# Kernel tuning notes

Hardware: AMD Instinct MI355X
Metric: run time of the kernel (lower is better)

The kernel has to match this reference:

```python
import jax, jax.numpy as jnp
import numpy as np

N = 50000      # nodes
E = 800000     # edges (avg degree 16)
F0 = 128       # input features
F = 128        # per-layer out_features (layer output = 2F after alpha/beta concat)
M = 16         # n_machines
BN_EPS = 1e-3  # Keras BatchNormalization default epsilon


def setup_inputs() -> dict:
    key = jax.random.key(0)
    ks = jax.random.split(key, 12)
    x = jax.random.normal(ks[0], (N, F0), jnp.float32)
    adj_rows = jax.random.randint(ks[1], (E,), 0, N, jnp.int32)
    adj_cols = jax.random.randint(ks[2], (E,), 0, N, jnp.int32)
    adj_vals = jax.random.uniform(ks[3], (E,), jnp.float32)
    l0_Walpha = jax.random.normal(ks[4], (6, F0, F), jnp.float32) * 0.05
    l0_Wbeta = jax.random.normal(ks[5], (6, F0, F), jnp.float32) * 0.05
    l0_bn = jax.random.normal(ks[6], (4, F), jnp.float32)
    l1_Walpha = jax.random.normal(ks[7], (6, 2 * F, F), jnp.float32) * 0.05
    l1_Wbeta = jax.random.normal(ks[8], (6, 2 * F, F), jnp.float32) * 0.05
    l1_bn = jax.random.normal(ks[9], (4, F), jnp.float32)
    We = jax.random.normal(ks[10], (2 * F, M), jnp.float32) * 0.05
    be = jax.random.normal(ks[11], (M,), jnp.float32) * 0.05
    return dict(x=x, adj_rows=adj_rows, adj_cols=adj_cols, adj_vals=adj_vals,
                l0_Walpha=l0_Walpha, l0_Wbeta=l0_Wbeta, l0_bn=l0_bn,
                l1_Walpha=l1_Walpha, l1_Wbeta=l1_Wbeta, l1_bn=l1_bn,
                We=We, be=be)


def _spmm(rows, cols, vals, x):
    # y[r] = sum_{edges (r,c)} vals * x[c]  == sparse A @ x
    return jax.ops.segment_sum(vals[:, None] * x[cols], rows, num_segments=x.shape[0])


def _bn(h, gamma, beta):
    # Keras BatchNormalization(axis=1) on (N, F): per-feature stats over nodes (training mode)
    mu = jnp.mean(h, axis=0, keepdims=True)
    var = jnp.var(h, axis=0, keepdims=True)
    return gamma * (h - mu) * jax.lax.rsqrt(var + BN_EPS) + beta


def _gnn_layer(x, rows, cols, vals, Wa, Wb, bn):
    a0 = _spmm(rows, cols, vals, x)
    a1 = _spmm(rows, cols, vals, a0)
    a2 = _spmm(rows, cols, vals, _spmm(rows, cols, vals, a1))
    alpha = x @ (Wa[0] + Wa[1] + Wa[2]) + a0 @ Wa[3] + a1 @ Wa[4] + a2 @ Wa[5]
    alpha = _bn(jax.nn.relu(alpha), bn[0], bn[1])
    beta = x @ (Wb[0] + Wb[1] + Wb[2]) + a0 @ Wb[3] + a1 @ Wb[4] + a2 @ Wb[5]
    beta = _bn(beta, bn[2], bn[3])
    return jnp.concatenate((alpha, beta), axis=1)  # (N, 2F)


def reference(x, adj_rows, adj_cols, adj_vals,
              l0_Walpha, l0_Wbeta, l0_bn,
              l1_Walpha, l1_Wbeta, l1_bn,
              We, be):
    h = _gnn_layer(x, adj_rows, adj_cols, adj_vals, l0_Walpha, l0_Wbeta, l0_bn)
    h = _gnn_layer(h, adj_rows, adj_cols, adj_vals, l1_Walpha, l1_Wbeta, l1_bn)
    # EdgeDense: per-edge score per machine = adj_val * (z[row] + z[col])
    z = h @ We + be                                   # (N, M)
    scores = adj_vals[:, None] * (z[adj_rows] + z[adj_cols])  # (E, M)
    return jax.nn.softmax(scores, axis=1)
```

## Files before the change

kernel.cpp:

```cpp
#include <hip/hip_runtime.h>
#include <stdint.h>

#define NN 50000
#define NE 800000
#define NP 50048
#define SCANB 196

typedef _Float16 f16x8 __attribute__((ext_vector_type(8)));
typedef float f32x4 __attribute__((ext_vector_type(4)));

__device__ __forceinline__ float h2f(unsigned short u){
  union { unsigned short u; _Float16 h; } x; x.u = u; return (float)x.h;
}
__device__ __forceinline__ unsigned short f2h(float f){
  union { _Float16 h; unsigned short u; } x; x.h = (_Float16)f; return x.u;
}
__device__ __forceinline__ void load_lds16(const void* g, void* l){
  __builtin_amdgcn_global_load_lds((const __attribute__((address_space(1))) void*)g,
                                   (__attribute__((address_space(3))) void*)l, 16, 0, 0);
}

__global__ void k_cast(const float* __restrict__ src, unsigned short* __restrict__ dst, int n4){
  int i = blockIdx.x*blockDim.x + threadIdx.x;
  if (i >= n4) return;
  float4 v = ((const float4*)src)[i];
  uint2 o;
  o.x = (unsigned int)f2h(v.x) | ((unsigned int)f2h(v.y) << 16);
  o.y = (unsigned int)f2h(v.z) | ((unsigned int)f2h(v.w) << 16);
  ((uint2*)dst)[i] = o;
}

__global__ void k_hist(const int* __restrict__ rows, int* __restrict__ cnt){
  int e = blockIdx.x*blockDim.x + threadIdx.x;
  if (e < NE) atomicAdd(&cnt[rows[e]], 1);
}

__global__ void k_scan1(const int* __restrict__ cnt, int* __restrict__ rowptr, int* __restrict__ bsum){
  __shared__ int sh[256];
  int t = threadIdx.x, b = blockIdx.x;
  int idx = b * 256 + t;
  int v = (idx < NN) ? cnt[idx] : 0;
  sh[t] = v; __syncthreads();
  #pragma unroll
  for (int off = 1; off < 256; off <<= 1){
    int u = (t >= off) ? sh[t - off] : 0;
    __syncthreads();
    sh[t] += u;
    __syncthreads();
  }
  if (idx < NN) rowptr[idx] = sh[t] - v;
  if (t == 255) bsum[b] = sh[255];
}

__global__ void k_scan2(const int* __restrict__ bsum, int* __restrict__ boff){
  __shared__ int sh[256];
  int t = threadIdx.x;
  int v = (t < SCANB) ? bsum[t] : 0;
  sh[t] = v; __syncthreads();
  #pragma unroll
  for (int off = 1; off < 256; off <<= 1){
    int u = (t >= off) ? sh[t - off] : 0;
    __syncthreads();
    sh[t] += u;
    __syncthreads();
  }
  if (t < SCANB) boff[t] = sh[t] - v;
  if (t == SCANB) boff[SCANB] = sh[255];
}

__global__ void k_scan3(int* __restrict__ rowptr, const int* __restrict__ boff){
  int idx = blockIdx.x * 256 + threadIdx.x;
  if (idx < NN) rowptr[idx] += boff[idx >> 8];
  else if (idx == NN) rowptr[NN] = boff[SCANB];
}

__global__ void k_scatter(const int* __restrict__ rows, const int* __restrict__ cols,
                          const float* __restrict__ vals,
                          const int* __restrict__ rowptr, int* __restrict__ fill,
                          int* __restrict__ colss, float* __restrict__ valss){
  int e = blockIdx.x*blockDim.x + threadIdx.x;
  if (e >= NE) return;
  int r = rows[e];
  int p = rowptr[r] + atomicAdd(&fill[r], 1);
  colss[p] = cols[e];
  valss[p] = vals[e];
}

__global__ void k_buildWT(const float* __restrict__ Wa, const float* __restrict__ Wb,
                          unsigned short* __restrict__ WT, int Fin){
  int Ktot = 4 * Fin;
  int idx = blockIdx.x*blockDim.x + threadIdx.x;
  if (idx >= 256 * Ktot) return;
  int j = idx / Ktot, k = idx - j * Ktot;
  int seg = k / Fin, ki = k - seg * Fin;
  const float* W = (j < 128) ? Wa : Wb;
  int jj = (j < 128) ? j : j - 128;
  int stride = Fin * 128;
  float v;
  if (seg == 0)
    v = W[0*stride + ki*128 + jj] + W[1*stride + ki*128 + jj] + W[2*stride + ki*128 + jj];
  else
    v = W[(seg + 2)*stride + ki*128 + jj];
  WT[j*Ktot + k] = f2h(v);
}

template<int F>
__global__ void k_spmm(const int* __restrict__ rowptr, const int* __restrict__ colss,
                       const float* __restrict__ valss,
                       const unsigned short* __restrict__ X, unsigned short* __restrict__ Y){
  int row = blockIdx.x * (blockDim.x >> 6) + (threadIdx.x >> 6);
  if (row >= NN) return;
  int lane = threadIdx.x & 63;
  constexpr int P = F / 64;
  float acc[P];
  #pragma unroll
  for (int i = 0; i < P; i++) acc[i] = 0.f;
  int s = rowptr[row], e = rowptr[row + 1];
  for (int base = s; base < e; base += 64){
    int idx = base + lane;
    bool ok = idx < e;
    int   cc = ok ? colss[idx] : 0;
    float vv = ok ? valss[idx] : 0.f;
    int n = e - base; if (n > 64) n = 64;
    for (int jb = 0; jb < n; jb += 8){
      int cj[8]; float vj[8];
      #pragma unroll
      for (int u = 0; u < 8; u++){
        cj[u] = __shfl(cc, jb + u);
        vj[u] = __shfl(vv, jb + u);
      }
      if (P == 2){
        unsigned int g[8];
        #pragma unroll
        for (int u = 0; u < 8; u++)
          g[u] = *(const unsigned int*)(X + (size_t)cj[u] * F + lane * P);
        #pragma unroll
        for (int u = 0; u < 8; u++){
          acc[0] += vj[u] * h2f((unsigned short)g[u]);
          acc[1] += vj[u] * h2f((unsigned short)(g[u] >> 16));
        }
      } else {
        uint2 g[8];
        #pragma unroll
        for (int u = 0; u < 8; u++)
          g[u] = *(const uint2*)(X + (size_t)cj[u] * F + lane * P);
        #pragma unroll
        for (int u = 0; u < 8; u++){
          acc[0] += vj[u] * h2f((unsigned short)g[u].x);
          acc[1] += vj[u] * h2f((unsigned short)(g[u].x >> 16));
          acc[2] += vj[u] * h2f((unsigned short)g[u].y);
          acc[3] += vj[u] * h2f((unsigned short)(g[u].y >> 16));
        }
      }
    }
  }
  unsigned short* dst = Y + (size_t)row * F + lane * P;
  if (P == 2){
    unsigned int o = (unsigned int)f2h(acc[0]) | ((unsigned int)f2h(acc[1]) << 16);
    *(unsigned int*)dst = o;
  } else {
    uint2 o;
    o.x = (unsigned int)f2h(acc[0]) | ((unsigned int)f2h(acc[1]) << 16);
    o.y = (unsigned int)f2h(acc[2]) | ((unsigned int)f2h(acc[3]) << 16);
    *(uint2*)dst = o;
  }
}

template<int FIN>
__global__ __launch_bounds__(256) void k_gemm4(
    const unsigned short* __restrict__ A0, const unsigned short* __restrict__ A1,
    const unsigned short* __restrict__ A2, const unsigned short* __restrict__ A3,
    const unsigned short* __restrict__ BT, float* __restrict__ C){
  constexpr int KTOT = 4 * FIN;
  __shared__ unsigned short As[128 * 32];
  __shared__ unsigned short Bs[128 * 32];
  int tid = threadIdx.x, lane = tid & 63;
  int wm = (tid >> 6) & 1, wn = tid >> 7;
  int bm = blockIdx.x, bn = blockIdx.y;

  f32x4 acc[4][4];
  #pragma unroll
  for (int i = 0; i < 4; i++)
    #pragma unroll
    for (int j = 0; j < 4; j++) acc[i][j] = (f32x4){0.f, 0.f, 0.f, 0.f};

  int ac = (tid & 3) * 8;
  int gr0 = bm * 128 + (tid >> 2);        if (gr0 >= NN) gr0 = NN - 1;
  int gr1 = bm * 128 + ((256 + tid) >> 2); if (gr1 >= NN) gr1 = NN - 1;
  int br0 = (tid >> 2), br1 = ((256 + tid) >> 2);
  const unsigned short* Bb = BT + (size_t)(bn * 128) * KTOT;
  unsigned short* Adst0 = As + (size_t)(tid & ~63) * 8;
  unsigned short* Adst1 = As + (size_t)(256 + (tid & ~63)) * 8;
  unsigned short* Bdst0 = Bs + (size_t)(tid & ~63) * 8;
  unsigned short* Bdst1 = Bs + (size_t)(256 + (tid & ~63)) * 8;

  int m0 = wm * 64 + (lane & 15);
  int n0 = wn * 64 + (lane & 15);
  int qk = (lane >> 4) * 8;

  #pragma unroll
  for (int seg = 0; seg < 4; seg++){
    const unsigned short* Asrc = (seg == 0) ? A0 : (seg == 1) ? A1 : (seg == 2) ? A2 : A3;
    const unsigned short* Bseg = Bb + seg * FIN;
    for (int kl = 0; kl < FIN; kl += 32){
      load_lds16(Asrc + (size_t)gr0 * FIN + kl + ac, Adst0);
      load_lds16(Asrc + (size_t)gr1 * FIN + kl + ac, Adst1);
      load_lds16(Bseg + (size_t)br0 * KTOT + kl + ac, Bdst0);
      load_lds16(Bseg + (size_t)br1 * KTOT + kl + ac, Bdst1);
      __syncthreads();
      f16x8 af[4], bfr[4];
      #pragma unroll
      for (int i = 0; i < 4; i++) af[i]  = *(const f16x8*)(As + (m0 + i * 16) * 32 + qk);
      #pragma unroll
      for (int j = 0; j < 4; j++) bfr[j] = *(const f16x8*)(Bs + (n0 + j * 16) * 32 + qk);
      #pragma unroll
      for (int i = 0; i < 4; i++)
        #pragma unroll
        for (int j = 0; j < 4; j++)
          acc[i][j] = __builtin_amdgcn_mfma_f32_16x16x32_f16(af[i], bfr[j], acc[i][j], 0, 0, 0);
      __syncthreads();
    }
  }
  int cn = bn * 128 + wn * 64 + (lane & 15);
  int rb = bm * 128 + wm * 64 + ((lane >> 4) << 2);
  #pragma unroll
  for (int i = 0; i < 4; i++)
    #pragma unroll
    for (int j = 0; j < 4; j++)
      #pragma unroll
      for (int g = 0; g < 4; g++){
        int rr = rb + i * 16 + g;
        if (rr < NN) C[(size_t)rr * 256 + cn + j * 16] = acc[i][j][g];
      }
}

__global__ void k_bnstats(const float* __restrict__ H, float* __restrict__ stats){
  int j = threadIdx.x;
  float s = 0.f, s2 = 0.f;
  for (int r = blockIdx.x; r < NN; r += gridDim.x){
    float v = H[(size_t)r * 256 + j];
    if (j < 128) v = fmaxf(v, 0.f);
    s += v; s2 += v * v;
  }
  atomicAdd(&stats[j], s);
  atomicAdd(&stats[256 + j], s2);
}

__global__ void k_bncoef(const float* __restrict__ stats, const float* __restrict__ bnp,
                         float* __restrict__ coef){
  int j = threadIdx.x;
  const float invN = 1.f / (float)NN;
  float mu = stats[j] * invN;
  float var = stats[256 + j] * invN - mu * mu;
  int jj = (j < 128) ? j : j - 128;
  float g = bnp[(j < 128 ? 0 : 2) * 128 + jj];
  float b = bnp[(j < 128 ? 1 : 3) * 128 + jj];
  float sc = g * rsqrtf(var + 1e-3f);
  coef[j] = sc;
  coef[256 + j] = b - mu * sc;
}

__global__ void k_bnapply(const float* __restrict__ H, const float* __restrict__ coef,
                          unsigned short* __restrict__ OUT){
  int j = threadIdx.x;
  float sc = coef[j], sh = coef[256 + j];
  for (int r = blockIdx.x; r < NN; r += gridDim.x){
    float v = H[(size_t)r * 256 + j];
    if (j < 128) v = fmaxf(v, 0.f);
    OUT[(size_t)r * 256 + j] = f2h(v * sc + sh);
  }
}

__global__ void k_bnzdense(const float* __restrict__ H, const float* __restrict__ coef,
                           const float* __restrict__ We, const float* __restrict__ be,
                           float* __restrict__ Z){
  __shared__ float Hs[16 * 256];
  __shared__ float Ws[256 * 16];
  int t = threadIdx.x;
  int r0 = blockIdx.x * 16;
  for (int i = t; i < 4096; i += 256){
    int col = i & 255;
    float v = H[(size_t)r0 * 256 + i];
    if (col < 128) v = fmaxf(v, 0.f);
    Hs[i] = v * coef[col] + coef[256 + col];
    Ws[i] = We[i];
  }
  __syncthreads();
  int r = t >> 4, m = t & 15;
  float accv = be[m];
  const float* hrow = Hs + r * 256;
  #pragma unroll 8
  for (int k = 0; k < 256; k++) accv += hrow[k] * Ws[k * 16 + m];
  Z[(size_t)(r0 + r) * 16 + m] = accv;
}

__global__ void k_edge(const int* __restrict__ rows, const int* __restrict__ cols,
                       const float* __restrict__ vals, const float* __restrict__ Z,
                       float* __restrict__ out){
  int e = blockIdx.x * blockDim.x + threadIdx.x;
  if (e >= NE) return;
  int r = rows[e], c = cols[e];
  float v = vals[e];
  const float4* zr = (const float4*)(Z + (size_t)r * 16);
  const float4* zc = (const float4*)(Z + (size_t)c * 16);
  float s[16];
  #pragma unroll
  for (int q = 0; q < 4; q++){
    float4 a = zr[q], b = zc[q];
    s[q * 4 + 0] = v * (a.x + b.x);
    s[q * 4 + 1] = v * (a.y + b.y);
    s[q * 4 + 2] = v * (a.z + b.z);
    s[q * 4 + 3] = v * (a.w + b.w);
  }
  float mx = s[0];
  #pragma unroll
  for (int i = 1; i < 16; i++) mx = fmaxf(mx, s[i]);
  float sum = 0.f;
  #pragma unroll
  for (int i = 0; i < 16; i++){ s[i] = __expf(s[i] - mx); sum += s[i]; }
  float inv = 1.f / sum;
  float4* po = (float4*)(out + (size_t)e * 16);
  #pragma unroll
  for (int q = 0; q < 4; q++)
    po[q] = make_float4(s[q*4+0]*inv, s[q*4+1]*inv, s[q*4+2]*inv, s[q*4+3]*inv);
}

extern "C" void kernel_launch(void* const* d_in, const int* in_sizes, int n_in,
                              void* d_out, int out_size, void* d_ws, size_t ws_size,
                              hipStream_t stream){
  const float* x    = (const float*)d_in[0];
  const int* rows   = (const int*)d_in[1];
  const int* cols   = (const int*)d_in[2];
  const float* vals = (const float*)d_in[3];
  const float* l0Wa = (const float*)d_in[4];
  const float* l0Wb = (const float*)d_in[5];
  const float* l0bn = (const float*)d_in[6];
  const float* l1Wa = (const float*)d_in[7];
  const float* l1Wb = (const float*)d_in[8];
  const float* l1bn = (const float*)d_in[9];
  const float* We   = (const float*)d_in[10];
  const float* be   = (const float*)d_in[11];
  float* out        = (float*)d_out;

  uint8_t* p = (uint8_t*)d_ws;
  auto take = [&](size_t b) -> void* { void* q = (void*)p; p += (b + 255) & ~(size_t)255; return q; };
  int*   rowptr = (int*)take((size_t)(NN + 1) * 4);
  int*   cnt    = (int*)take((size_t)NN * 4);
  int*   fill   = (int*)take((size_t)NN * 4);
  int*   bsum   = (int*)take((size_t)SCANB * 4);
  int*   boff   = (int*)take((size_t)(SCANB + 1) * 4);
  int*   colss  = (int*)take((size_t)NE * 4);
  float* valss  = (float*)take((size_t)NE * 4);
  unsigned short* WT0 = (unsigned short*)take((size_t)256 * 512 * 2);
  unsigned short* WT1 = (unsigned short*)take((size_t)256 * 1024 * 2);
  float* stats  = (float*)take(512 * 4);
  float* coef   = (float*)take(512 * 4);
  float* Z      = (float*)take((size_t)NN * 16 * 4);
  float* Hpre   = (float*)take((size_t)NN * 256 * 4);
  unsigned short* x16 = (unsigned short*)take((size_t)NN * 128 * 2);
  unsigned short* buf[5];
  for (int i = 0; i < 5; i++) buf[i] = (unsigned short*)take((size_t)NN * 256 * 2);

  hipMemsetAsync(cnt, 0, (size_t)NN * 4, stream);
  hipMemsetAsync(fill, 0, (size_t)NN * 4, stream);
  k_hist<<<NE / 256, 256, 0, stream>>>(rows, cnt);
  k_scan1<<<SCANB, 256, 0, stream>>>(cnt, rowptr, bsum);
  k_scan2<<<1, 256, 0, stream>>>(bsum, boff);
  k_scan3<<<SCANB, 256, 0, stream>>>(rowptr, boff);
  k_scatter<<<NE / 256, 256, 0, stream>>>(rows, cols, vals, rowptr, fill, colss, valss);
  k_buildWT<<<(256 * 512) / 256, 256, 0, stream>>>(l0Wa, l0Wb, WT0, 128);
  k_buildWT<<<(256 * 1024) / 256, 256, 0, stream>>>(l1Wa, l1Wb, WT1, 256);
  k_cast<<<(NN * 128 / 4 + 255) / 256, 256, 0, stream>>>(x, x16, NN * 128 / 4);

  dim3 gg(NP / 128, 2);

  k_spmm<128><<<NN / 4, 256, 0, stream>>>(rowptr, colss, valss, x16,    buf[0]);
  k_spmm<128><<<NN / 4, 256, 0, stream>>>(rowptr, colss, valss, buf[0], buf[1]);
  k_spmm<128><<<NN / 4, 256, 0, stream>>>(rowptr, colss, valss, buf[1], buf[2]);
  k_spmm<128><<<NN / 4, 256, 0, stream>>>(rowptr, colss, valss, buf[2], buf[3]);
  k_gemm4<128><<<gg, 256, 0, stream>>>(x16, buf[0], buf[1], buf[3], WT0, Hpre);
  hipMemsetAsync(stats, 0, 512 * 4, stream);
  k_bnstats<<<512, 256, 0, stream>>>(Hpre, stats);
  k_bncoef<<<1, 256, 0, stream>>>(stats, l0bn, coef);
  k_bnapply<<<2048, 256, 0, stream>>>(Hpre, coef, buf[4]);

  k_spmm<256><<<NN / 4, 256, 0, stream>>>(rowptr, colss, valss, buf[4], buf[0]);
  k_spmm<256><<<NN / 4, 256, 0, stream>>>(rowptr, colss, valss, buf[0], buf[1]);
  k_spmm<256><<<NN / 4, 256, 0, stream>>>(rowptr, colss, valss, buf[1], buf[2]);
  k_spmm<256><<<NN / 4, 256, 0, stream>>>(rowptr, colss, valss, buf[2], buf[3]);
  k_gemm4<256><<<gg, 256, 0, stream>>>(buf[4], buf[0], buf[1], buf[3], WT1, Hpre);
  hipMemsetAsync(stats, 0, 512 * 4, stream);
  k_bnstats<<<512, 256, 0, stream>>>(Hpre, stats);
  k_bncoef<<<1, 256, 0, stream>>>(stats, l1bn, coef);
  k_bnzdense<<<NN / 16, 256, 0, stream>>>(Hpre, coef, We, be, Z);

  k_edge<<<NE / 256, 256, 0, stream>>>(rows, cols, vals, Z, out);
}
```

Baseline: 777.2 us.

## Fuse BN statistics into GEMM epilogue, store fp16 pre-activations, merge scan kernels

The GEMM epilogue now writes fp16 pre-activations and reduces per-column sum and sum-of-squares into the stats buffer with wave shuffles plus atomics. This removes the separate stats pass and the coef kernel, and halves the Hpre traffic. The BN coefficients are recomputed per block inside bnapply and bnzdense, and the two scan fixup kernels are merged into one. SpMM now unrolls the edge gather 16 wide instead of 8 for more memory-level parallelism. The trade-offs are fp16 rounding of the pre-BN values, plus padded lanes issuing extra loads when a row's degree is not a multiple of 16.

Measured after the change: 758.4 us. 2.4% less time.

```diff
diff --git a/kernel.cpp b/kernel.cpp
--- a/kernel.cpp
+++ b/kernel.cpp
@@ -52,9 +52,9 @@
   if (t == 255) bsum[b] = sh[255];
 }
 
-__global__ void k_scan2(const int* __restrict__ bsum, int* __restrict__ boff){
+__global__ void k_scan3(int* __restrict__ rowptr, const int* __restrict__ bsum){
   __shared__ int sh[256];
-  int t = threadIdx.x;
+  int t = threadIdx.x, b = blockIdx.x;
   int v = (t < SCANB) ? bsum[t] : 0;
   sh[t] = v; __syncthreads();
   #pragma unroll
@@ -64,14 +64,11 @@
     sh[t] += u;
     __syncthreads();
   }
-  if (t < SCANB) boff[t] = sh[t] - v;
-  if (t == SCANB) boff[SCANB] = sh[255];
-}
-
-__global__ void k_scan3(int* __restrict__ rowptr, const int* __restrict__ boff){
-  int idx = blockIdx.x * 256 + threadIdx.x;
-  if (idx < NN) rowptr[idx] += boff[idx >> 8];
-  else if (idx == NN) rowptr[NN] = boff[SCANB];
+  int boffb = (b == 0) ? 0 : sh[b - 1];
+  int total = sh[SCANB - 1];
+  int idx = b * 256 + t;
+  if (idx < NN) rowptr[idx] += boffb;
+  else if (idx == NN) rowptr[NN] = total;
 }
 
 __global__ void k_scatter(const int* __restrict__ rows, const int* __restrict__ cols,
@@ -122,30 +119,31 @@
     int   cc = ok ? colss[idx] : 0;
     float vv = ok ? valss[idx] : 0.f;
     int n = e - base; if (n > 64) n = 64;
-    for (int jb = 0; jb < n; jb += 8){
-      int cj[8]; float vj[8];
+    int nr = (n + 15) & ~15;
+    for (int jb = 0; jb < nr; jb += 16){
+      int cj[16]; float vj[16];
       #pragma unroll
-      for (int u = 0; u < 8; u++){
+      for (int u = 0; u < 16; u++){
         cj[u] = __shfl(cc, jb + u);
         vj[u] = __shfl(vv, jb + u);
       }
       if (P == 2){
-        unsigned int g[8];
+        unsigned int g[16];
         #pragma unroll
-        for (int u = 0; u < 8; u++)
+        for (int u = 0; u < 16; u++)
           g[u] = *(const unsigned int*)(X + (size_t)cj[u] * F + lane * P);
         #pragma unroll
-        for (int u = 0; u < 8; u++){
+        for (int u = 0; u < 16; u++){
           acc[0] += vj[u] * h2f((unsigned short)g[u]);
           acc[1] += vj[u] * h2f((unsigned short)(g[u] >> 16));
         }
       } else {
-        uint2 g[8];
+        uint2 g[16];
         #pragma unroll
-        for (int u = 0; u < 8; u++)
+        for (int u = 0; u < 16; u++)
           g[u] = *(const uint2*)(X + (size_t)cj[u] * F + lane * P);
         #pragma unroll
-        for (int u = 0; u < 8; u++){
+        for (int u = 0; u < 16; u++){
           acc[0] += vj[u] * h2f((unsigned short)g[u].x);
           acc[1] += vj[u] * h2f((unsigned short)(g[u].x >> 16));
           acc[2] += vj[u] * h2f((unsigned short)g[u].y);
@@ -170,7 +168,8 @@
 __global__ __launch_bounds__(256) void k_gemm4(
     const unsigned short* __restrict__ A0, const unsigned short* __restrict__ A1,
     const unsigned short* __restrict__ A2, const unsigned short* __restrict__ A3,
-    const unsigned short* __restrict__ BT, float* __restrict__ C){
+    const unsigned short* __restrict__ BT, unsigned short* __restrict__ Hp,
+    float* __restrict__ stats){
   constexpr int KTOT = 4 * FIN;
   __shared__ unsigned short As[128 * 32];
   __shared__ unsigned short Bs[128 * 32];
@@ -221,68 +220,89 @@
       __syncthreads();
     }
   }
-  int cn = bn * 128 + wn * 64 + (lane & 15);
-  int rb = bm * 128 + wm * 64 + ((lane >> 4) << 2);
-  #pragma unroll
-  for (int i = 0; i < 4; i++)
+  int cnb = bn * 128 + wn * 64 + (lane & 15);
+  int rb  = bm * 128 + wm * 64 + ((lane >> 4) << 2);
+  float sj[4], qj[4];
+  #pragma unroll
+  for (int j = 0; j < 4; j++){
+    float sv = 0.f, qv = 0.f;
     #pragma unroll
-    for (int j = 0; j < 4; j++)
+    for (int i = 0; i < 4; i++)
       #pragma unroll
       for (int g = 0; g < 4; g++){
         int rr = rb + i * 16 + g;
-        if (rr < NN) C[(size_t)rr * 256 + cn + j * 16] = acc[i][j][g];
+        float val = acc[i][j][g];
+        bool okr = rr < NN;
+        if (okr) Hp[(size_t)rr * 256 + cnb + j * 16] = f2h(val);
+        float v = okr ? val : 0.f;
+        if (bn == 0) v = fmaxf(v, 0.f);
+        sv += v; qv += v * v;
       }
-}
-
-__global__ void k_bnstats(const float* __restrict__ H, float* __restrict__ stats){
-  int j = threadIdx.x;
-  float s = 0.f, s2 = 0.f;
+    sj[j] = sv; qj[j] = qv;
+  }
+  #pragma unroll
+  for (int j = 0; j < 4; j++){
+    sj[j] += __shfl_xor(sj[j], 16); sj[j] += __shfl_xor(sj[j], 32);
+    qj[j] += __shfl_xor(qj[j], 16); qj[j] += __shfl_xor(qj[j], 32);
+  }
+  if (lane < 16){
+    #pragma unroll
+    for (int j = 0; j < 4; j++){
+      int c = bn * 128 + wn * 64 + j * 16 + lane;
+      atomicAdd(&stats[c], sj[j]);
+      atomicAdd(&stats[256 + c], qj[j]);
+    }
+  }
+}
+
+__global__ void k_bnapply(const unsigned short* __restrict__ Hp, const float* __restrict__ stats,
+                          const float* __restrict__ bnp, unsigned short* __restrict__ OUT){
+  __shared__ float scs[256], sbs[256];
+  int t = threadIdx.x;
+  {
+    const float invN = 1.f / (float)NN;
+    float mu = stats[t] * invN;
+    float var = stats[256 + t] * invN - mu * mu;
+    int jj = (t < 128) ? t : t - 128;
+    float g = bnp[(t < 128 ? 0 : 2) * 128 + jj];
+    float b = bnp[(t < 128 ? 1 : 3) * 128 + jj];
+    float sc = g * rsqrtf(var + 1e-3f);
+    scs[t] = sc; sbs[t] = b - mu * sc;
+  }
+  __syncthreads();
+  float sc = scs[t], sh = sbs[t];
   for (int r = blockIdx.x; r < NN; r += gridDim.x){
-    float v = H[(size_t)r * 256 + j];
-    if (j < 128) v = fmaxf(v, 0.f);
-    s += v; s2 += v * v;
-  }
-  atomicAdd(&stats[j], s);
-  atomicAdd(&stats[256 + j], s2);
-}
-
-__global__ void k_bncoef(const float* __restrict__ stats, const float* __restrict__ bnp,
-                         float* __restrict__ coef){
-  int j = threadIdx.x;
-  const float invN = 1.f / (float)NN;
-  float mu = stats[j] * invN;
-  float var = stats[256 + j] * invN - mu * mu;
-  int jj = (j < 128) ? j : j - 128;
-  float g = bnp[(j < 128 ? 0 : 2) * 128 + jj];
-  float b = bnp[(j < 128 ? 1 : 3) * 128 + jj];
-  float sc = g * rsqrtf(var + 1e-3f);
-  coef[j] = sc;
-  coef[256 + j] = b - mu * sc;
-}
-
-__global__ void k_bnapply(const float* __restrict__ H, const float* __restrict__ coef,
-                          unsigned short* __restrict__ OUT){
-  int j = threadIdx.x;
-  float sc = coef[j], sh = coef[256 + j];
-  for (int r = blockIdx.x; r < NN; r += gridDim.x){
-    float v = H[(size_t)r * 256 + j];
-    if (j < 128) v = fmaxf(v, 0.f);
-    OUT[(size_t)r * 256 + j] = f2h(v * sc + sh);
-  }
-}
-
-__global__ void k_bnzdense(const float* __restrict__ H, const float* __restrict__ coef,
+    float v = h2f(Hp[(size_t)r * 256 + t]);
+    if (t < 128) v = fmaxf(v, 0.f);
+    OUT[(size_t)r * 256 + t] = f2h(v * sc + sh);
+  }
+}
+
+__global__ void k_bnzdense(const unsigned short* __restrict__ Hp, const float* __restrict__ stats,
+                           const float* __restrict__ bnp,
                            const float* __restrict__ We, const float* __restrict__ be,
                            float* __restrict__ Z){
   __shared__ float Hs[16 * 256];
   __shared__ float Ws[256 * 16];
+  __shared__ float scs[256], sbs[256];
   int t = threadIdx.x;
+  {
+    const float invN = 1.f / (float)NN;
+    float mu = stats[t] * invN;
+    float var = stats[256 + t] * invN - mu * mu;
+    int jj = (t < 128) ? t : t - 128;
+    float g = bnp[(t < 128 ? 0 : 2) * 128 + jj];
+    float b = bnp[(t < 128 ? 1 : 3) * 128 + jj];
+    float sc = g * rsqrtf(var + 1e-3f);
+    scs[t] = sc; sbs[t] = b - mu * sc;
+  }
+  __syncthreads();
   int r0 = blockIdx.x * 16;
   for (int i = t; i < 4096; i += 256){
     int col = i & 255;
-    float v = H[(size_t)r0 * 256 + i];
+    float v = h2f(Hp[(size_t)r0 * 256 + i]);
     if (col < 128) v = fmaxf(v, 0.f);
-    Hs[i] = v * coef[col] + coef[256 + col];
+    Hs[i] = v * scs[col] + sbs[col];
     Ws[i] = We[i];
   }
   __syncthreads();
@@ -348,15 +368,13 @@
   int*   cnt    = (int*)take((size_t)NN * 4);
   int*   fill   = (int*)take((size_t)NN * 4);
   int*   bsum   = (int*)take((size_t)SCANB * 4);
-  int*   boff   = (int*)take((size_t)(SCANB + 1) * 4);
   int*   colss  = (int*)take((size_t)NE * 4);
   float* valss  = (float*)take((size_t)NE * 4);
   unsigned short* WT0 = (unsigned short*)take((size_t)256 * 512 * 2);
   unsigned short* WT1 = (unsigned short*)take((size_t)256 * 1024 * 2);
   float* stats  = (float*)take(512 * 4);
-  float* coef   = (float*)take(512 * 4);
   float* Z      = (float*)take((size_t)NN * 16 * 4);
-  float* Hpre   = (float*)take((size_t)NN * 256 * 4);
+  unsigned short* Hp  = (unsigned short*)take((size_t)NN * 256 * 2);
   unsigned short* x16 = (unsigned short*)take((size_t)NN * 128 * 2);
   unsigned short* buf[5];
   for (int i = 0; i < 5; i++) buf[i] = (unsigned short*)take((size_t)NN * 256 * 2);
@@ -365,8 +383,7 @@
   hipMemsetAsync(fill, 0, (size_t)NN * 4, stream);
   k_hist<<<NE / 256, 256, 0, stream>>>(rows, cnt);
   k_scan1<<<SCANB, 256, 0, stream>>>(cnt, rowptr, bsum);
-  k_scan2<<<1, 256, 0, stream>>>(bsum, boff);
-  k_scan3<<<SCANB, 256, 0, stream>>>(rowptr, boff);
+  k_scan3<<<SCANB, 256, 0, stream>>>(rowptr, bsum);
   k_scatter<<<NE / 256, 256, 0, stream>>>(rows, cols, vals, rowptr, fill, colss, valss);
   k_buildWT<<<(256 * 512) / 256, 256, 0, stream>>>(l0Wa, l0Wb, WT0, 128);
   k_buildWT<<<(256 * 1024) / 256, 256, 0, stream>>>(l1Wa, l1Wb, WT1, 256);
@@ -378,21 +395,17 @@
   k_spmm<128><<<NN / 4, 256, 0, stream>>>(rowptr, colss, valss, buf[0], buf[1]);
   k_spmm<128><<<NN / 4, 256, 0, stream>>>(rowptr, colss, valss, buf[1], buf[2]);
   k_spmm<128><<<NN / 4, 256, 0, stream>>>(rowptr, colss, valss, buf[2], buf[3]);
-  k_gemm4<128><<<gg, 256, 0, stream>>>(x16, buf[0], buf[1], buf[3], WT0, Hpre);
   hipMemsetAsync(stats, 0, 512 * 4, stream);
-  k_bnstats<<<512, 256, 0, stream>>>(Hpre, stats);
-  k_bncoef<<<1, 256, 0, stream>>>(stats, l0bn, coef);
-  k_bnapply<<<2048, 256, 0, stream>>>(Hpre, coef, buf[4]);
+  k_gemm4<128><<<gg, 256, 0, stream>>>(x16, buf[0], buf[1], buf[3], WT0, Hp, stats);
+  k_bnapply<<<2048, 256, 0, stream>>>(Hp, stats, l0bn, buf[4]);
 
   k_spmm<256><<<NN / 4, 256, 0, stream>>>(rowptr, colss, valss, buf[4], buf[0]);
   k_spmm<256><<<NN / 4, 256, 0, stream>>>(rowptr, colss, valss, buf[0], buf[1]);
   k_spmm<256><<<NN / 4, 256, 0, stream>>>(rowptr, colss, valss, buf[1], buf[2]);
   k_spmm<256><<<NN / 4, 256, 0, stream>>>(rowptr, colss, valss, buf[2], buf[3]);
-  k_gemm4<256><<<gg, 256, 0, stream>>>(buf[4], buf[0], buf[1], buf[3], WT1, Hpre);
   hipMemsetAsync(stats, 0, 512 * 4, stream);
-  k_bnstats<<<512, 256, 0, stream>>>(Hpre, stats);
-  k_bncoef<<<1, 256, 0, stream>>>(stats, l1bn, coef);
-  k_bnzdense<<<NN / 16, 256, 0, stream>>>(Hpre, coef, We, be, Z);
+  k_gemm4<256><<<gg, 256, 0, stream>>>(buf[4], buf[0], buf[1], buf[3], WT1, Hp, stats);
+  k_bnzdense<<<NN / 16, 256, 0, stream>>>(Hp, stats, l1bn, We, be, Z);
 
   k_edge<<<NE / 256, 256, 0, stream>>>(rows, cols, vals, Z, out);
 }
```
